# Kernel tuning notes

Measured on AMD Instinct MI355X. Metric: run time of the kernel, lower is better.

Reference implementation:

```python
import jax, jax.numpy as jnp
import numpy as np

B, L, D, N = 32, 2048, 1024, 16
N_ITERS = 4
EPS = 1e-8
RMS_EPS = 1e-6
H = 2 * D  # SwiGLU hidden


def setup_inputs() -> dict:
    key = jax.random.key(0)
    ks = jax.random.split(key, 16)
    w = lambda i, shape: jax.random.normal(ks[i], shape, dtype=jnp.float32) * 0.02
    return {
        "encoder_output": jax.random.normal(ks[0], (B, L, D), dtype=jnp.float32),
        "slots_noise": jax.random.normal(ks[1], (B, N, D), dtype=jnp.float32),
        "slots_mu": w(2, (1, 1, D)),
        "slots_sigma": jnp.abs(w(3, (1, 1, D))),
        "g_in": jnp.ones((D,), jnp.float32),     # norm_input.weight
        "g_slots": jnp.ones((D,), jnp.float32),  # norm_slots.weight
        "Wq": w(4, (D, D)),   # torch Linear weight layout (out, in)
        "Wk": w(5, (D, D)),
        "Wv": w(6, (D, D)),
        "w1": w(7, (H, D)),
        "w2": w(8, (H, D)),
        "w3": w(9, (D, H)),
        "W_ih": w(10, (3 * D, D)),  # GRUCell weight_ih (r,z,n stacked)
        "W_hh": w(11, (3 * D, D)),
        "b_ih": jnp.zeros((3 * D,), jnp.float32),
        "b_hh": jnp.zeros((3 * D,), jnp.float32),
    }


def _rmsnorm(x, g):
    var = jnp.mean(x * x, axis=-1, keepdims=True)
    return x * jax.lax.rsqrt(var + RMS_EPS) * g


def _gru_cell(x, h, W_ih, W_hh, b_ih, b_hh):
    # torch.nn.GRUCell: gates ordered (r, z, n)
    gi = x @ W_ih.T + b_ih   # [..., 3D]
    gh = h @ W_hh.T + b_hh
    gi_r, gi_z, gi_n = jnp.split(gi, 3, axis=-1)
    gh_r, gh_z, gh_n = jnp.split(gh, 3, axis=-1)
    r = jax.nn.sigmoid(gi_r + gh_r)
    z = jax.nn.sigmoid(gi_z + gh_z)
    n = jnp.tanh(gi_n + r * gh_n)
    return (1.0 - z) * n + z * h


def reference(encoder_output, slots_noise, slots_mu, slots_sigma, g_in, g_slots,
              Wq, Wk, Wv, w1, w2, w3, W_ih, W_hh, b_ih, b_hh):
    d = encoder_output.shape[-1]
    scale = d ** (-0.5)

    inputs = _rmsnorm(encoder_output, g_in)          # [B, L, D]
    k = inputs @ Wk.T                                # [B, L, D]
    v = inputs @ Wv.T                                # [B, L, D]

    slots = slots_mu + slots_sigma * slots_noise     # [B, N, D]

    for _ in range(N_ITERS):
        slots_prev = slots
        s = _rmsnorm(slots, g_slots)                 # [B, N, D]
        q = s @ Wq.T                                 # [B, N, D]
        dots = jnp.einsum('bnd,bld->bnl', q, k) * scale   # [B, N, L]
        attn = jax.nn.softmax(dots, axis=1)          # competitive softmax over slots
        updates = jnp.einsum('bnl,bld->bnd', attn + EPS, v)     # [B, N, D]
        updates = updates / (jnp.sum(attn, axis=-1, keepdims=True) + EPS)
        # SwiGLU
        updates = (jax.nn.silu(updates @ w1.T) * (updates @ w2.T)) @ w3.T
        slots = _gru_cell(updates, slots_prev, W_ih, W_hh, b_ih, b_hh)
    return slots
```

## Files before the change

### kernel.cpp

```cpp
#include <hip/hip_runtime.h>
#include <hip/hip_bf16.h>
#include <stdint.h>


typedef __bf16 bf16;
typedef __bf16 bf16x2 __attribute__((ext_vector_type(2)));
typedef __bf16 bf16x4 __attribute__((ext_vector_type(4)));
typedef __bf16 bf16x8 __attribute__((ext_vector_type(8)));
typedef float  f32x4  __attribute__((ext_vector_type(4)));

#define MFMA16(a,b,c) __builtin_amdgcn_mfma_f32_16x16x32_bf16((a),(b),(c),0,0,0)

__device__ __forceinline__ void gload16(const void* g, void* l) {
  __builtin_amdgcn_global_load_lds((__attribute__((address_space(1))) const void*)g,
                                   (__attribute__((address_space(3))) void*)l, 16, 0, 0);
}

template<int OUT_F32>
__global__ __launch_bounds__(256, 4)
void gemm_bt64(const bf16* __restrict__ A0, const bf16* __restrict__ B0, void* __restrict__ C0,
               const bf16* __restrict__ A1, const bf16* __restrict__ B1, void* __restrict__ C1,
               int N, int K, float* zbuf)
{
  if (zbuf != nullptr && blockIdx.x == 0 && blockIdx.y == 0 && blockIdx.z == 0) {
    zbuf[threadIdx.x] = 0.f;
    zbuf[threadIdx.x + 256] = 0.f;
  }
  const bf16* A = blockIdx.z ? A1 : A0;
  const bf16* B = blockIdx.z ? B1 : B0;
  void* C = blockIdx.z ? C1 : C0;
  __shared__ __align__(16) bf16 As[64 * 64];
  __shared__ __align__(16) bf16 Bs[64 * 64];
  const int tid = threadIdx.x, wave = tid >> 6, lane = tid & 63;
  const int wm = wave >> 1, wn = wave & 1;
  const int brow = blockIdx.y * 64, bcol = blockIdx.x * 64;
  const int r8 = lane >> 3, c8 = (lane & 7) * 8;
  const int cl = lane & 15, rh = lane >> 4;
  f32x4 acc[2][2] = {};

  for (int k0 = 0; k0 < K; k0 += 64) {
    __syncthreads();
    gload16(A + (size_t)(brow + wave * 16 + r8) * K + k0 + c8,     &As[(wave * 16) * 64]);
    gload16(A + (size_t)(brow + wave * 16 + 8 + r8) * K + k0 + c8, &As[(wave * 16 + 8) * 64]);
    gload16(B + (size_t)(bcol + wave * 16 + r8) * K + k0 + c8,     &Bs[(wave * 16) * 64]);
    gload16(B + (size_t)(bcol + wave * 16 + 8 + r8) * K + k0 + c8, &Bs[(wave * 16 + 8) * 64]);
    __syncthreads();
#pragma unroll
    for (int kk = 0; kk < 2; ++kk) {
      bf16x8 af[2], bfv[2];
#pragma unroll
      for (int m = 0; m < 2; ++m)
        af[m] = *(const bf16x8*)&As[(wm * 32 + m * 16 + cl) * 64 + kk * 32 + rh * 8];
#pragma unroll
      for (int n = 0; n < 2; ++n)
        bfv[n] = *(const bf16x8*)&Bs[(wn * 32 + n * 16 + cl) * 64 + kk * 32 + rh * 8];
#pragma unroll
      for (int m = 0; m < 2; ++m)
#pragma unroll
        for (int n = 0; n < 2; ++n)
          acc[m][n] = MFMA16(af[m], bfv[n], acc[m][n]);
    }
  }
#pragma unroll
  for (int m = 0; m < 2; ++m)
#pragma unroll
    for (int n = 0; n < 2; ++n) {
      int row0 = brow + wm * 32 + m * 16 + rh * 4;
      int col  = bcol + wn * 32 + n * 16 + cl;
#pragma unroll
      for (int r = 0; r < 4; ++r) {
        if (OUT_F32) ((float*)C)[(size_t)(row0 + r) * N + col] = acc[m][n][r];
        else         ((bf16*)C)[(size_t)(row0 + r) * N + col] = (bf16)acc[m][n][r];
      }
    }
}

__global__ __launch_bounds__(256, 4)
void gemm_swiglu(const bf16* __restrict__ A, const bf16* __restrict__ B12, bf16* __restrict__ G)
{
  __shared__ __align__(16) bf16 As[64 * 64];
  __shared__ __align__(16) bf16 B1s[64 * 64];
  __shared__ __align__(16) bf16 B2s[64 * 64];
  const int tid = threadIdx.x, wave = tid >> 6, lane = tid & 63;
  const int wm = wave >> 1, wn = wave & 1;
  const int brow = blockIdx.y * 64, bcol = blockIdx.x * 64;
  const int r8 = lane >> 3, c8 = (lane & 7) * 8;
  const int cl = lane & 15, rh = lane >> 4;
  f32x4 acc1[2][2] = {}, acc2[2][2] = {};

  for (int k0 = 0; k0 < 1024; k0 += 64) {
    __syncthreads();
    gload16(A   + (size_t)(brow + wave * 16 + r8) * 1024 + k0 + c8,            &As[(wave * 16) * 64]);
    gload16(A   + (size_t)(brow + wave * 16 + 8 + r8) * 1024 + k0 + c8,        &As[(wave * 16 + 8) * 64]);
    gload16(B12 + (size_t)(bcol + wave * 16 + r8) * 1024 + k0 + c8,            &B1s[(wave * 16) * 64]);
    gload16(B12 + (size_t)(bcol + wave * 16 + 8 + r8) * 1024 + k0 + c8,        &B1s[(wave * 16 + 8) * 64]);
    gload16(B12 + (size_t)(2048 + bcol + wave * 16 + r8) * 1024 + k0 + c8,     &B2s[(wave * 16) * 64]);
    gload16(B12 + (size_t)(2048 + bcol + wave * 16 + 8 + r8) * 1024 + k0 + c8, &B2s[(wave * 16 + 8) * 64]);
    __syncthreads();
#pragma unroll
    for (int kk = 0; kk < 2; ++kk) {
      bf16x8 af[2], b1v[2], b2v[2];
#pragma unroll
      for (int m = 0; m < 2; ++m)
        af[m] = *(const bf16x8*)&As[(wm * 32 + m * 16 + cl) * 64 + kk * 32 + rh * 8];
#pragma unroll
      for (int n = 0; n < 2; ++n) {
        b1v[n] = *(const bf16x8*)&B1s[(wn * 32 + n * 16 + cl) * 64 + kk * 32 + rh * 8];
        b2v[n] = *(const bf16x8*)&B2s[(wn * 32 + n * 16 + cl) * 64 + kk * 32 + rh * 8];
      }
#pragma unroll
      for (int m = 0; m < 2; ++m)
#pragma unroll
        for (int n = 0; n < 2; ++n) {
          acc1[m][n] = MFMA16(af[m], b1v[n], acc1[m][n]);
          acc2[m][n] = MFMA16(af[m], b2v[n], acc2[m][n]);
        }
    }
  }
#pragma unroll
  for (int m = 0; m < 2; ++m)
#pragma unroll
    for (int n = 0; n < 2; ++n) {
      int row0 = brow + wm * 32 + m * 16 + rh * 4;
      int col  = bcol + wn * 32 + n * 16 + cl;
#pragma unroll
      for (int r = 0; r < 4; ++r) {
        float h1 = acc1[m][n][r], h2 = acc2[m][n][r];
        G[(size_t)(row0 + r) * 2048 + col] = (bf16)(h1 / (1.f + __expf(-h1)) * h2);
      }
    }
}

__global__ __launch_bounds__(256, 2)
void fused_attn(const bf16* __restrict__ qm, const bf16* __restrict__ x,
                float* __restrict__ part, float* __restrict__ attn_sum)
{
  extern __shared__ __align__(16) char smem[];
  char* ss  = smem;
  char* ksl = smem + 32768;
  float* p_lds = (float*)(smem + 65536);

  const int lc = blockIdx.x, b = blockIdx.y;
  const int tid = threadIdx.x, wave = tid >> 6, lane = tid & 63;
  const int cl = lane & 15, rh = lane >> 4;

  const bf16* sb = qm + (size_t)b * 16 * 1024;
  {
    const int c16 = tid & 127, row2 = tid >> 7;
#pragma unroll
    for (int i = 0; i < 8; ++i) {
      int row = i * 2 + row2;
      int colb = (c16 * 16) ^ ((row & 7) << 4);
      gload16(sb + row * 1024 + colb / 2, ss + i * 4096 + wave * 1024);
    }
  }

  const bf16* kb = x + ((size_t)b * 2048 + lc * 128) * 1024;
  const int ksw  = ((lane & 7) ^ ((lane >> 3) & 7)) * 8;
  const int krow = wave * 8 + (lane >> 3);

#define STAGE_KS(KT) {                                                            \
    char* d_ = ksl + ((KT) & 1) * 16384;                                          \
    _Pragma("unroll")                                                             \
    for (int i = 0; i < 4; ++i)                                                   \
      gload16(kb + (size_t)(i * 32 + krow) * 1024 + (KT) * 64 + ksw,              \
              d_ + (i * 32 + wave * 8) * 128);                                    \
  }

  f32x4 acc[2] = {};
  STAGE_KS(0)
  for (int kt = 0; kt < 16; ++kt) {
    if (kt < 15) { STAGE_KS(kt + 1) }
    __builtin_amdgcn_sched_barrier(0);
    if (kt < 15) asm volatile("s_waitcnt vmcnt(4)" ::: "memory");
    else         asm volatile("s_waitcnt vmcnt(0)" ::: "memory");
    __builtin_amdgcn_sched_barrier(0);
    __builtin_amdgcn_s_barrier();
    const char* sbuf = ksl + (kt & 1) * 16384;
#pragma unroll
    for (int kk = 0; kk < 2; ++kk) {
      bf16x8 af = *(const bf16x8*)(ss + cl * 2048 +
                    ((kt * 128 + kk * 64 + rh * 16) ^ ((cl & 7) << 4)));
#pragma unroll
      for (int n = 0; n < 2; ++n) {
        int row = wave * 32 + n * 16 + cl;
        bf16x8 bfv = *(const bf16x8*)(sbuf + row * 128 +
                      ((kk * 64 + rh * 16) ^ ((row & 7) << 4)));
        acc[n] = MFMA16(af, bfv, acc[n]);
      }
    }
    __builtin_amdgcn_s_barrier();
    __builtin_amdgcn_sched_barrier(0);
  }
#undef STAGE_KS

  const float scale = 0.03125f;
  float rs[4] = {0.f, 0.f, 0.f, 0.f};
#pragma unroll
  for (int n = 0; n < 2; ++n) {
    float xv[4];
#pragma unroll
    for (int r = 0; r < 4; ++r) xv[r] = acc[n][r] * scale;
    float mx = fmaxf(fmaxf(xv[0], xv[1]), fmaxf(xv[2], xv[3]));
    mx = fmaxf(mx, __shfl_xor(mx, 16));
    mx = fmaxf(mx, __shfl_xor(mx, 32));
    float e[4], sm = 0.f;
#pragma unroll
    for (int r = 0; r < 4; ++r) { e[r] = __expf(xv[r] - mx); sm += e[r]; }
    sm += __shfl_xor(sm, 16);
    sm += __shfl_xor(sm, 32);
    float inv = 1.f / sm;
    f32x4 pk;
#pragma unroll
    for (int r = 0; r < 4; ++r) { float av = e[r] * inv; rs[r] += av; pk[r] = av; }
    int ll = wave * 32 + n * 16 + cl;
    *(f32x4*)&p_lds[ll * 20 + rh * 4] = pk;
  }
#pragma unroll
  for (int off = 1; off < 16; off <<= 1) {
#pragma unroll
    for (int r = 0; r < 4; ++r) rs[r] += __shfl_xor(rs[r], off);
  }
  if (cl == 0) {
#pragma unroll
    for (int r = 0; r < 4; ++r) atomicAdd(&attn_sum[b * 16 + rh * 4 + r], rs[r]);
  }
  __syncthreads();

  const bf16* vb = x + ((size_t)b * 2048 + lc * 128) * 1024 + tid * 4;
  float pacc[16][4] = {};
  for (int l = 0; l < 128; ++l) {
    bf16x4 vv = *(const bf16x4*)(vb + (size_t)l * 1024);
    float vf0 = (float)vv[0], vf1 = (float)vv[1], vf2 = (float)vv[2], vf3 = (float)vv[3];
    float pv[16];
    *(f32x4*)&pv[0]  = *(const f32x4*)&p_lds[l * 20];
    *(f32x4*)&pv[4]  = *(const f32x4*)&p_lds[l * 20 + 4];
    *(f32x4*)&pv[8]  = *(const f32x4*)&p_lds[l * 20 + 8];
    *(f32x4*)&pv[12] = *(const f32x4*)&p_lds[l * 20 + 12];
#pragma unroll
    for (int n = 0; n < 16; ++n) {
      pacc[n][0] += pv[n] * vf0; pacc[n][1] += pv[n] * vf1;
      pacc[n][2] += pv[n] * vf2; pacc[n][3] += pv[n] * vf3;
    }
  }
  float* pb = part + ((size_t)(lc * 32 + b) * 16) * 1024 + tid * 4;
#pragma unroll
  for (int n = 0; n < 16; ++n)
    *(f32x4*)(pb + (size_t)n * 1024) = *(f32x4*)&pacc[n][0];
}

__global__ void updates_finalize(const float* __restrict__ part, const float* __restrict__ attn_sum,
                                 bf16* __restrict__ updraw)
{
  int idx = blockIdx.x * 256 + threadIdx.x;
  int m = idx >> 10;
  float sm = 0.f;
#pragma unroll
  for (int ls = 0; ls < 16; ++ls) sm += part[idx + (size_t)ls * 524288];
  updraw[idx] = (bf16)(sm / (attn_sum[m] + 1e-8f));
}

__global__ __launch_bounds__(256)
void gru_pw_fused(const float* __restrict__ gi, const float* __restrict__ gh,
                  const float* __restrict__ bih, const float* __restrict__ bhh,
                  const float* __restrict__ g_sl,
                  float* __restrict__ slots, bf16* __restrict__ slots_bf,
                  bf16* __restrict__ s_bf, float* __restrict__ outp)
{
  const int m = blockIdx.x, tid = threadIdx.x;
  const int d0 = tid * 4;
  const size_t base = (size_t)m * 3072 + d0;
  f32x4 gir = *(const f32x4*)(gi + base),        ghr = *(const f32x4*)(gh + base);
  f32x4 giz = *(const f32x4*)(gi + base + 1024), ghz = *(const f32x4*)(gh + base + 1024);
  f32x4 gin = *(const f32x4*)(gi + base + 2048), ghn = *(const f32x4*)(gh + base + 2048);
  f32x4 br  = *(const f32x4*)(bih + d0),        bhr = *(const f32x4*)(bhh + d0);
  f32x4 bz  = *(const f32x4*)(bih + 1024 + d0), bhz = *(const f32x4*)(bhh + 1024 + d0);
  f32x4 bn  = *(const f32x4*)(bih + 2048 + d0), bhn = *(const f32x4*)(bhh + 2048 + d0);
  f32x4 h   = *(const f32x4*)(slots + (size_t)m * 1024 + d0);
  float o[4]; float ssum = 0.f;
#pragma unroll
  for (int j = 0; j < 4; ++j) {
    float r  = gir[j] + br[j] + ghr[j] + bhr[j];
    float z  = giz[j] + bz[j] + ghz[j] + bhz[j];
    float nn = gin[j] + bn[j];
    float hn = ghn[j] + bhn[j];
    r = 1.f / (1.f + expf(-r));
    z = 1.f / (1.f + expf(-z));
    nn = tanhf(nn + r * hn);
    o[j] = (1.f - z) * nn + z * h[j];
    ssum += o[j] * o[j];
  }
#pragma unroll
  for (int off = 32; off; off >>= 1) ssum += __shfl_xor(ssum, off);
  __shared__ float red[4];
  if ((tid & 63) == 0) red[tid >> 6] = ssum;
  __syncthreads();
  float tot = red[0] + red[1] + red[2] + red[3];
  float rsc = rsqrtf(tot * (1.f / 1024.f) + 1e-6f);
  f32x4 gv = *(const f32x4*)(g_sl + d0);
  f32x4 of; bf16x4 ob, sb;
#pragma unroll
  for (int j = 0; j < 4; ++j) { of[j] = o[j]; ob[j] = (bf16)o[j]; sb[j] = (bf16)(o[j] * rsc * gv[j]); }
  *(f32x4*)(slots + (size_t)m * 1024 + d0) = of;
  *(f32x4*)(outp  + (size_t)m * 1024 + d0) = of;
  *(bf16x4*)(slots_bf + (size_t)m * 1024 + d0) = ob;
  *(bf16x4*)(s_bf     + (size_t)m * 1024 + d0) = sb;
}

__global__ __launch_bounds__(256)
void init_slots_fused(const float* __restrict__ noise, const float* __restrict__ mu,
                      const float* __restrict__ sigma, const float* __restrict__ g_sl,
                      float* __restrict__ slots, bf16* __restrict__ slots_bf,
                      bf16* __restrict__ s_bf)
{
  const int m = blockIdx.x, tid = threadIdx.x;
  const int d0 = tid * 4;
  f32x4 nz = *(const f32x4*)(noise + (size_t)m * 1024 + d0);
  f32x4 mv = *(const f32x4*)(mu + d0);
  f32x4 sg = *(const f32x4*)(sigma + d0);
  float o[4]; float ssum = 0.f;
#pragma unroll
  for (int j = 0; j < 4; ++j) { o[j] = mv[j] + sg[j] * nz[j]; ssum += o[j] * o[j]; }
#pragma unroll
  for (int off = 32; off; off >>= 1) ssum += __shfl_xor(ssum, off);
  __shared__ float red[4];
  if ((tid & 63) == 0) red[tid >> 6] = ssum;
  __syncthreads();
  float tot = red[0] + red[1] + red[2] + red[3];
  float rsc = rsqrtf(tot * (1.f / 1024.f) + 1e-6f);
  f32x4 gv = *(const f32x4*)(g_sl + d0);
  f32x4 of; bf16x4 ob, sb;
#pragma unroll
  for (int j = 0; j < 4; ++j) { of[j] = o[j]; ob[j] = (bf16)o[j]; sb[j] = (bf16)(o[j] * rsc * gv[j]); }
  *(f32x4*)(slots + (size_t)m * 1024 + d0) = of;
  *(bf16x4*)(slots_bf + (size_t)m * 1024 + d0) = ob;
  *(bf16x4*)(s_bf     + (size_t)m * 1024 + d0) = sb;
}

__global__ __launch_bounds__(256)
void rmsnorm_cast(const float* __restrict__ x, const float* __restrict__ g, bf16* __restrict__ y)
{
  const int row = blockIdx.x, tid = threadIdx.x;
  float4 xv = ((const float4*)(x + (size_t)row * 1024))[tid];
  float ss = xv.x * xv.x + xv.y * xv.y + xv.z * xv.z + xv.w * xv.w;
#pragma unroll
  for (int off = 32; off; off >>= 1) ss += __shfl_xor(ss, off);
  __shared__ float red[4];
  if ((tid & 63) == 0) red[tid >> 6] = ss;
  __syncthreads();
  float tot = red[0] + red[1] + red[2] + red[3];
  float rs = rsqrtf(tot * (1.f / 1024.f) + 1e-6f);
  float4 gv = ((const float4*)g)[tid];
  bf16x4 o;
  o[0] = (bf16)(xv.x * rs * gv.x); o[1] = (bf16)(xv.y * rs * gv.y);
  o[2] = (bf16)(xv.z * rs * gv.z); o[3] = (bf16)(xv.w * rs * gv.w);
  *(bf16x4*)(y + (size_t)row * 1024 + tid * 4) = o;
}

__global__ __launch_bounds__(256)
void transpose_cast(const float* __restrict__ in, bf16* __restrict__ out)
{
  __shared__ float tile[32][33];
  const int bx = blockIdx.x * 32, by = blockIdx.y * 32;
  const int tx = threadIdx.x & 31, ty = threadIdx.x >> 5;
#pragma unroll
  for (int i = 0; i < 32; i += 8)
    tile[ty + i][tx] = in[(size_t)(by + ty + i) * 1024 + bx + tx];
  __syncthreads();
#pragma unroll
  for (int i = 0; i < 32; i += 8)
    out[(size_t)(bx + ty + i) * 1024 + by + tx] = (bf16)tile[tx][ty + i];
}

__global__ void cast_bf16_x4(const float* __restrict__ x, bf16* __restrict__ y)
{
  int i = (blockIdx.x * 256 + threadIdx.x) * 4;
  float4 v = *(const float4*)(x + i);
  bf16x4 o; o[0] = (bf16)v.x; o[1] = (bf16)v.y; o[2] = (bf16)v.z; o[3] = (bf16)v.w;
  *(bf16x4*)(y + i) = o;
}

extern "C" void kernel_launch(void* const* d_in, const int* in_sizes, int n_in,
                              void* d_out, int out_size, void* d_ws, size_t ws_size,
                              hipStream_t stream)
{
  const float* enc    = (const float*)d_in[0];
  const float* noise  = (const float*)d_in[1];
  const float* mu     = (const float*)d_in[2];
  const float* sigma  = (const float*)d_in[3];
  const float* g_in   = (const float*)d_in[4];
  const float* g_sl   = (const float*)d_in[5];
  const float* Wq     = (const float*)d_in[6];
  const float* Wk     = (const float*)d_in[7];
  const float* Wv     = (const float*)d_in[8];
  const float* w1     = (const float*)d_in[9];
  const float* w2     = (const float*)d_in[10];
  const float* w3     = (const float*)d_in[11];
  const float* Wih    = (const float*)d_in[12];
  const float* Whh    = (const float*)d_in[13];
  const float* bih    = (const float*)d_in[14];
  const float* bhh    = (const float*)d_in[15];

  char* p = (char*)d_ws;
  auto alloc = [&](size_t bytes) { char* r = p; p += (bytes + 255) & ~(size_t)255; return (void*)r; };

  bf16* inputs  = (bf16*)alloc((size_t)32 * 2048 * 1024 * 2);
  bf16* qm_w    = (bf16*)alloc((size_t)1024 * 1024 * 2);
  bf16* wv_b    = (bf16*)alloc((size_t)1024 * 1024 * 2);
  bf16* wqT_b   = (bf16*)alloc((size_t)1024 * 1024 * 2);
  bf16* wkT_b   = (bf16*)alloc((size_t)1024 * 1024 * 2);
  bf16* w12_b   = (bf16*)alloc((size_t)4096 * 1024 * 2);
  bf16* w3_b    = (bf16*)alloc((size_t)1024 * 2048 * 2);
  bf16* wih_b   = (bf16*)alloc((size_t)3072 * 1024 * 2);
  bf16* whh_b   = (bf16*)alloc((size_t)3072 * 1024 * 2);
  float* slots  = (float*)alloc(512 * 1024 * 4);
  bf16* slots_bf= (bf16*)alloc(512 * 1024 * 2);
  bf16* s_bf    = (bf16*)alloc(512 * 1024 * 2);
  bf16* qm_bf   = (bf16*)alloc(512 * 1024 * 2);
  float* attn_sum = (float*)alloc(32 * 16 * 4);
  float* part   = (float*)alloc((size_t)16 * 512 * 1024 * 4);
  bf16* updraw  = (bf16*)alloc(512 * 1024 * 2);
  bf16* upd_bf  = (bf16*)alloc(512 * 1024 * 2);
  bf16* g_bf    = (bf16*)alloc((size_t)512 * 2048 * 2);
  bf16* swout   = (bf16*)alloc(512 * 1024 * 2);
  float* gif    = (float*)alloc((size_t)512 * 3072 * 4);
  float* ghf    = (float*)alloc((size_t)512 * 3072 * 4);

  transpose_cast<<<dim3(32, 32), 256, 0, stream>>>(Wq, wqT_b);
  transpose_cast<<<dim3(32, 32), 256, 0, stream>>>(Wk, wkT_b);
  gemm_bt64<0><<<dim3(16, 16, 1), 256, 0, stream>>>(wkT_b, wqT_b, qm_w, wkT_b, wqT_b, qm_w, 1024, 1024, nullptr);
  cast_bf16_x4<<<1024, 256, 0, stream>>>(Wv, wv_b);
  cast_bf16_x4<<<2048, 256, 0, stream>>>(w1, w12_b);
  cast_bf16_x4<<<2048, 256, 0, stream>>>(w2, w12_b + (size_t)2048 * 1024);
  cast_bf16_x4<<<2048, 256, 0, stream>>>(w3, w3_b);
  cast_bf16_x4<<<3072, 256, 0, stream>>>(Wih, wih_b);
  cast_bf16_x4<<<3072, 256, 0, stream>>>(Whh, whh_b);

  rmsnorm_cast<<<65536, 256, 0, stream>>>(enc, g_in, inputs);
  init_slots_fused<<<512, 256, 0, stream>>>(noise, mu, sigma, g_sl, slots, slots_bf, s_bf);

  hipFuncSetAttribute(reinterpret_cast<const void*>(fused_attn),
                      hipFuncAttributeMaxDynamicSharedMemorySize, 75776);

  for (int it = 0; it < 4; ++it) {
    gemm_bt64<0><<<dim3(16, 8, 1), 256, 0, stream>>>(s_bf, qm_w, qm_bf, s_bf, qm_w, qm_bf, 1024, 1024, attn_sum);
    fused_attn<<<dim3(16, 32), 256, 75776, stream>>>(qm_bf, inputs, part, attn_sum);
    updates_finalize<<<2048, 256, 0, stream>>>(part, attn_sum, updraw);
    gemm_bt64<0><<<dim3(16, 8, 1), 256, 0, stream>>>(updraw, wv_b, upd_bf, updraw, wv_b, upd_bf, 1024, 1024, nullptr);
    gemm_swiglu<<<dim3(32, 8), 256, 0, stream>>>(upd_bf, w12_b, g_bf);
    gemm_bt64<0><<<dim3(16, 8, 1), 256, 0, stream>>>(g_bf, w3_b, swout, g_bf, w3_b, swout, 1024, 2048, nullptr);
    gemm_bt64<1><<<dim3(48, 8, 2), 256, 0, stream>>>(swout, wih_b, gif, slots_bf, whh_b, ghf, 3072, 1024, nullptr);
    float* outp = (it == 3) ? (float*)d_out : slots;
    gru_pw_fused<<<512, 256, 0, stream>>>(gif, ghf, bih, bhh, g_sl, slots, slots_bf, s_bf, outp);
  }
}
```

Baseline: 796.6 us.

## Fold Wv and w3 into neighbouring weights and double-buffer GEMM LDS

Precomputes the weight products (w1;w2)·Wv and W_ih·w3 once per call so each iteration drops two small GEMM launches: the Wv projection merges into the SwiGLU GEMM, and the w3 projection merges into the GRU input GEMM with K=2048. Both GEMM kernels also switch to double-buffered LDS tiles, prefetching the next K-tile while computing the current one, with explicit vmcnt waits and barriers. The cost is three extra setup GEMMs, more per-iteration K work in the GRU GEMM, fewer blocks per CU for the SwiGLU kernel, and changed bf16 rounding because the weights are pre-multiplied.

New measurement: 735.3 us. -7.7%, faster.

```diff
diff --git a/kernel.cpp b/kernel.cpp
--- a/kernel.cpp
+++ b/kernel.cpp
@@ -4,7 +4,6 @@
 
 
 typedef __bf16 bf16;
-typedef __bf16 bf16x2 __attribute__((ext_vector_type(2)));
 typedef __bf16 bf16x4 __attribute__((ext_vector_type(4)));
 typedef __bf16 bf16x8 __attribute__((ext_vector_type(8)));
 typedef float  f32x4  __attribute__((ext_vector_type(4)));
@@ -20,7 +19,7 @@
 __global__ __launch_bounds__(256, 4)
 void gemm_bt64(const bf16* __restrict__ A0, const bf16* __restrict__ B0, void* __restrict__ C0,
                const bf16* __restrict__ A1, const bf16* __restrict__ B1, void* __restrict__ C1,
-               int N, int K, float* zbuf)
+               int N, int K0, int K1, float* zbuf)
 {
   if (zbuf != nullptr && blockIdx.x == 0 && blockIdx.y == 0 && blockIdx.z == 0) {
     zbuf[threadIdx.x] = 0.f;
@@ -29,8 +28,9 @@
   const bf16* A = blockIdx.z ? A1 : A0;
   const bf16* B = blockIdx.z ? B1 : B0;
   void* C = blockIdx.z ? C1 : C0;
-  __shared__ __align__(16) bf16 As[64 * 64];
-  __shared__ __align__(16) bf16 Bs[64 * 64];
+  const int K = blockIdx.z ? K1 : K0;
+  __shared__ __align__(16) bf16 As[2][64 * 64];
+  __shared__ __align__(16) bf16 Bs[2][64 * 64];
   const int tid = threadIdx.x, wave = tid >> 6, lane = tid & 63;
   const int wm = wave >> 1, wn = wave & 1;
   const int brow = blockIdx.y * 64, bcol = blockIdx.x * 64;
@@ -38,29 +38,53 @@
   const int cl = lane & 15, rh = lane >> 4;
   f32x4 acc[2][2] = {};
 
-  for (int k0 = 0; k0 < K; k0 += 64) {
-    __syncthreads();
-    gload16(A + (size_t)(brow + wave * 16 + r8) * K + k0 + c8,     &As[(wave * 16) * 64]);
-    gload16(A + (size_t)(brow + wave * 16 + 8 + r8) * K + k0 + c8, &As[(wave * 16 + 8) * 64]);
-    gload16(B + (size_t)(bcol + wave * 16 + r8) * K + k0 + c8,     &Bs[(wave * 16) * 64]);
-    gload16(B + (size_t)(bcol + wave * 16 + 8 + r8) * K + k0 + c8, &Bs[(wave * 16 + 8) * 64]);
-    __syncthreads();
+  const bf16* pa0 = A + (size_t)(brow + wave * 16 + r8) * K + c8;
+  const bf16* pa1 = A + (size_t)(brow + wave * 16 + 8 + r8) * K + c8;
+  const bf16* pb0 = B + (size_t)(bcol + wave * 16 + r8) * K + c8;
+  const bf16* pb1 = B + (size_t)(bcol + wave * 16 + 8 + r8) * K + c8;
+
+#define ST64(T) {                                                   \
+    int k0_ = (T) * 64, s_ = (T) & 1;                               \
+    gload16(pa0 + k0_, &As[s_][(wave * 16) * 64]);                  \
+    gload16(pa1 + k0_, &As[s_][(wave * 16 + 8) * 64]);              \
+    gload16(pb0 + k0_, &Bs[s_][(wave * 16) * 64]);                  \
+    gload16(pb1 + k0_, &Bs[s_][(wave * 16 + 8) * 64]);              \
+  }
+
+  const int nt = K >> 6;
+  ST64(0)
+  for (int t = 0; t < nt; ++t) {
+    if (t + 1 < nt) {
+      ST64(t + 1)
+      asm volatile("s_waitcnt vmcnt(4)" ::: "memory");
+    } else {
+      asm volatile("s_waitcnt vmcnt(0)" ::: "memory");
+    }
+    __builtin_amdgcn_sched_barrier(0);
+    __builtin_amdgcn_s_barrier();
+    __builtin_amdgcn_sched_barrier(0);
+    const int s = t & 1;
 #pragma unroll
     for (int kk = 0; kk < 2; ++kk) {
       bf16x8 af[2], bfv[2];
 #pragma unroll
       for (int m = 0; m < 2; ++m)
-        af[m] = *(const bf16x8*)&As[(wm * 32 + m * 16 + cl) * 64 + kk * 32 + rh * 8];
+        af[m] = *(const bf16x8*)&As[s][(wm * 32 + m * 16 + cl) * 64 + kk * 32 + rh * 8];
 #pragma unroll
       for (int n = 0; n < 2; ++n)
-        bfv[n] = *(const bf16x8*)&Bs[(wn * 32 + n * 16 + cl) * 64 + kk * 32 + rh * 8];
+        bfv[n] = *(const bf16x8*)&Bs[s][(wn * 32 + n * 16 + cl) * 64 + kk * 32 + rh * 8];
 #pragma unroll
       for (int m = 0; m < 2; ++m)
 #pragma unroll
         for (int n = 0; n < 2; ++n)
           acc[m][n] = MFMA16(af[m], bfv[n], acc[m][n]);
     }
-  }
+    __builtin_amdgcn_sched_barrier(0);
+    __builtin_amdgcn_s_barrier();
+    __builtin_amdgcn_sched_barrier(0);
+  }
+#undef ST64
+
 #pragma unroll
   for (int m = 0; m < 2; ++m)
 #pragma unroll
@@ -75,12 +99,12 @@
     }
 }
 
-__global__ __launch_bounds__(256, 4)
+__global__ __launch_bounds__(256, 3)
 void gemm_swiglu(const bf16* __restrict__ A, const bf16* __restrict__ B12, bf16* __restrict__ G)
 {
-  __shared__ __align__(16) bf16 As[64 * 64];
-  __shared__ __align__(16) bf16 B1s[64 * 64];
-  __shared__ __align__(16) bf16 B2s[64 * 64];
+  __shared__ __align__(16) bf16 As[2][64 * 64];
+  __shared__ __align__(16) bf16 B1s[2][64 * 64];
+  __shared__ __align__(16) bf16 B2s[2][64 * 64];
   const int tid = threadIdx.x, wave = tid >> 6, lane = tid & 63;
   const int wm = wave >> 1, wn = wave & 1;
   const int brow = blockIdx.y * 64, bcol = blockIdx.x * 64;
@@ -88,25 +112,45 @@
   const int cl = lane & 15, rh = lane >> 4;
   f32x4 acc1[2][2] = {}, acc2[2][2] = {};
 
-  for (int k0 = 0; k0 < 1024; k0 += 64) {
-    __syncthreads();
-    gload16(A   + (size_t)(brow + wave * 16 + r8) * 1024 + k0 + c8,            &As[(wave * 16) * 64]);
-    gload16(A   + (size_t)(brow + wave * 16 + 8 + r8) * 1024 + k0 + c8,        &As[(wave * 16 + 8) * 64]);
-    gload16(B12 + (size_t)(bcol + wave * 16 + r8) * 1024 + k0 + c8,            &B1s[(wave * 16) * 64]);
-    gload16(B12 + (size_t)(bcol + wave * 16 + 8 + r8) * 1024 + k0 + c8,        &B1s[(wave * 16 + 8) * 64]);
-    gload16(B12 + (size_t)(2048 + bcol + wave * 16 + r8) * 1024 + k0 + c8,     &B2s[(wave * 16) * 64]);
-    gload16(B12 + (size_t)(2048 + bcol + wave * 16 + 8 + r8) * 1024 + k0 + c8, &B2s[(wave * 16 + 8) * 64]);
-    __syncthreads();
+  const bf16* pa0 = A   + (size_t)(brow + wave * 16 + r8) * 1024 + c8;
+  const bf16* pa1 = A   + (size_t)(brow + wave * 16 + 8 + r8) * 1024 + c8;
+  const bf16* p10 = B12 + (size_t)(bcol + wave * 16 + r8) * 1024 + c8;
+  const bf16* p11 = B12 + (size_t)(bcol + wave * 16 + 8 + r8) * 1024 + c8;
+  const bf16* p20 = B12 + (size_t)(2048 + bcol + wave * 16 + r8) * 1024 + c8;
+  const bf16* p21 = B12 + (size_t)(2048 + bcol + wave * 16 + 8 + r8) * 1024 + c8;
+
+#define STSW(T) {                                                   \
+    int k0_ = (T) * 64, s_ = (T) & 1;                               \
+    gload16(pa0 + k0_, &As[s_][(wave * 16) * 64]);                  \
+    gload16(pa1 + k0_, &As[s_][(wave * 16 + 8) * 64]);              \
+    gload16(p10 + k0_, &B1s[s_][(wave * 16) * 64]);                 \
+    gload16(p11 + k0_, &B1s[s_][(wave * 16 + 8) * 64]);             \
+    gload16(p20 + k0_, &B2s[s_][(wave * 16) * 64]);                 \
+    gload16(p21 + k0_, &B2s[s_][(wave * 16 + 8) * 64]);             \
+  }
+
+  STSW(0)
+  for (int t = 0; t < 16; ++t) {
+    if (t < 15) {
+      STSW(t + 1)
+      asm volatile("s_waitcnt vmcnt(6)" ::: "memory");
+    } else {
+      asm volatile("s_waitcnt vmcnt(0)" ::: "memory");
+    }
+    __builtin_amdgcn_sched_barrier(0);
+    __builtin_amdgcn_s_barrier();
+    __builtin_amdgcn_sched_barrier(0);
+    const int s = t & 1;
 #pragma unroll
     for (int kk = 0; kk < 2; ++kk) {
       bf16x8 af[2], b1v[2], b2v[2];
 #pragma unroll
       for (int m = 0; m < 2; ++m)
-        af[m] = *(const bf16x8*)&As[(wm * 32 + m * 16 + cl) * 64 + kk * 32 + rh * 8];
+        af[m] = *(const bf16x8*)&As[s][(wm * 32 + m * 16 + cl) * 64 + kk * 32 + rh * 8];
 #pragma unroll
       for (int n = 0; n < 2; ++n) {
-        b1v[n] = *(const bf16x8*)&B1s[(wn * 32 + n * 16 + cl) * 64 + kk * 32 + rh * 8];
-        b2v[n] = *(const bf16x8*)&B2s[(wn * 32 + n * 16 + cl) * 64 + kk * 32 + rh * 8];
+        b1v[n] = *(const bf16x8*)&B1s[s][(wn * 32 + n * 16 + cl) * 64 + kk * 32 + rh * 8];
+        b2v[n] = *(const bf16x8*)&B2s[s][(wn * 32 + n * 16 + cl) * 64 + kk * 32 + rh * 8];
       }
 #pragma unroll
       for (int m = 0; m < 2; ++m)
@@ -116,7 +160,12 @@
           acc2[m][n] = MFMA16(af[m], b2v[n], acc2[m][n]);
         }
     }
-  }
+    __builtin_amdgcn_sched_barrier(0);
+    __builtin_amdgcn_s_barrier();
+    __builtin_amdgcn_sched_barrier(0);
+  }
+#undef STSW
+
 #pragma unroll
   for (int m = 0; m < 2; ++m)
 #pragma unroll
@@ -358,18 +407,18 @@
 }
 
 __global__ __launch_bounds__(256)
-void transpose_cast(const float* __restrict__ in, bf16* __restrict__ out)
+void transpose_cast(const float* __restrict__ in, bf16* __restrict__ out, int R, int C)
 {
   __shared__ float tile[32][33];
   const int bx = blockIdx.x * 32, by = blockIdx.y * 32;
   const int tx = threadIdx.x & 31, ty = threadIdx.x >> 5;
 #pragma unroll
   for (int i = 0; i < 32; i += 8)
-    tile[ty + i][tx] = in[(size_t)(by + ty + i) * 1024 + bx + tx];
+    tile[ty + i][tx] = in[(size_t)(by + ty + i) * C + bx + tx];
   __syncthreads();
 #pragma unroll
   for (int i = 0; i < 32; i += 8)
-    out[(size_t)(bx + ty + i) * 1024 + by + tx] = (bf16)tile[tx][ty + i];
+    out[(size_t)(bx + ty + i) * R + by + tx] = (bf16)tile[tx][ty + i];
 }
 
 __global__ void cast_bf16_x4(const float* __restrict__ x, bf16* __restrict__ y)
@@ -406,12 +455,14 @@
 
   bf16* inputs  = (bf16*)alloc((size_t)32 * 2048 * 1024 * 2);
   bf16* qm_w    = (bf16*)alloc((size_t)1024 * 1024 * 2);
-  bf16* wv_b    = (bf16*)alloc((size_t)1024 * 1024 * 2);
   bf16* wqT_b   = (bf16*)alloc((size_t)1024 * 1024 * 2);
   bf16* wkT_b   = (bf16*)alloc((size_t)1024 * 1024 * 2);
-  bf16* w12_b   = (bf16*)alloc((size_t)4096 * 1024 * 2);
-  bf16* w3_b    = (bf16*)alloc((size_t)1024 * 2048 * 2);
-  bf16* wih_b   = (bf16*)alloc((size_t)3072 * 1024 * 2);
+  bf16* wvT_b   = (bf16*)alloc((size_t)1024 * 1024 * 2);
+  bf16* w3T_b   = (bf16*)alloc((size_t)2048 * 1024 * 2);
+  bf16* w12_bf  = (bf16*)alloc((size_t)4096 * 1024 * 2);
+  bf16* w12v    = (bf16*)alloc((size_t)4096 * 1024 * 2);
+  bf16* wih_bf  = (bf16*)alloc((size_t)3072 * 1024 * 2);
+  bf16* wih3_b  = (bf16*)alloc((size_t)3072 * 2048 * 2);
   bf16* whh_b   = (bf16*)alloc((size_t)3072 * 1024 * 2);
   float* slots  = (float*)alloc(512 * 1024 * 4);
   bf16* slots_bf= (bf16*)alloc(512 * 1024 * 2);
@@ -420,21 +471,24 @@
   float* attn_sum = (float*)alloc(32 * 16 * 4);
   float* part   = (float*)alloc((size_t)16 * 512 * 1024 * 4);
   bf16* updraw  = (bf16*)alloc(512 * 1024 * 2);
-  bf16* upd_bf  = (bf16*)alloc(512 * 1024 * 2);
   bf16* g_bf    = (bf16*)alloc((size_t)512 * 2048 * 2);
-  bf16* swout   = (bf16*)alloc(512 * 1024 * 2);
   float* gif    = (float*)alloc((size_t)512 * 3072 * 4);
   float* ghf    = (float*)alloc((size_t)512 * 3072 * 4);
 
-  transpose_cast<<<dim3(32, 32), 256, 0, stream>>>(Wq, wqT_b);
-  transpose_cast<<<dim3(32, 32), 256, 0, stream>>>(Wk, wkT_b);
-  gemm_bt64<0><<<dim3(16, 16, 1), 256, 0, stream>>>(wkT_b, wqT_b, qm_w, wkT_b, wqT_b, qm_w, 1024, 1024, nullptr);
-  cast_bf16_x4<<<1024, 256, 0, stream>>>(Wv, wv_b);
-  cast_bf16_x4<<<2048, 256, 0, stream>>>(w1, w12_b);
-  cast_bf16_x4<<<2048, 256, 0, stream>>>(w2, w12_b + (size_t)2048 * 1024);
-  cast_bf16_x4<<<2048, 256, 0, stream>>>(w3, w3_b);
-  cast_bf16_x4<<<3072, 256, 0, stream>>>(Wih, wih_b);
+  transpose_cast<<<dim3(32, 32), 256, 0, stream>>>(Wq, wqT_b, 1024, 1024);
+  transpose_cast<<<dim3(32, 32), 256, 0, stream>>>(Wk, wkT_b, 1024, 1024);
+  transpose_cast<<<dim3(32, 32), 256, 0, stream>>>(Wv, wvT_b, 1024, 1024);
+  transpose_cast<<<dim3(64, 32), 256, 0, stream>>>(w3, w3T_b, 1024, 2048);
+  cast_bf16_x4<<<2048, 256, 0, stream>>>(w1, w12_bf);
+  cast_bf16_x4<<<2048, 256, 0, stream>>>(w2, w12_bf + (size_t)2048 * 1024);
+  cast_bf16_x4<<<3072, 256, 0, stream>>>(Wih, wih_bf);
   cast_bf16_x4<<<3072, 256, 0, stream>>>(Whh, whh_b);
+  gemm_bt64<0><<<dim3(16, 16, 1), 256, 0, stream>>>(wkT_b, wqT_b, qm_w, wkT_b, wqT_b, qm_w,
+                                                    1024, 1024, 1024, nullptr);
+  gemm_bt64<0><<<dim3(16, 64, 1), 256, 0, stream>>>(w12_bf, wvT_b, w12v, w12_bf, wvT_b, w12v,
+                                                    1024, 1024, 1024, nullptr);
+  gemm_bt64<0><<<dim3(32, 48, 1), 256, 0, stream>>>(wih_bf, w3T_b, wih3_b, wih_bf, w3T_b, wih3_b,
+                                                    2048, 1024, 1024, nullptr);
 
   rmsnorm_cast<<<65536, 256, 0, stream>>>(enc, g_in, inputs);
   init_slots_fused<<<512, 256, 0, stream>>>(noise, mu, sigma, g_sl, slots, slots_bf, s_bf);
@@ -443,13 +497,13 @@
                       hipFuncAttributeMaxDynamicSharedMemorySize, 75776);
 
   for (int it = 0; it < 4; ++it) {
-    gemm_bt64<0><<<dim3(16, 8, 1), 256, 0, stream>>>(s_bf, qm_w, qm_bf, s_bf, qm_w, qm_bf, 1024, 1024, attn_sum);
+    gemm_bt64<0><<<dim3(16, 8, 1), 256, 0, stream>>>(s_bf, qm_w, qm_bf, s_bf, qm_w, qm_bf,
+                                                     1024, 1024, 1024, attn_sum);
     fused_attn<<<dim3(16, 32), 256, 75776, stream>>>(qm_bf, inputs, part, attn_sum);
     updates_finalize<<<2048, 256, 0, stream>>>(part, attn_sum, updraw);
-    gemm_bt64<0><<<dim3(16, 8, 1), 256, 0, stream>>>(updraw, wv_b, upd_bf, updraw, wv_b, upd_bf, 1024, 1024, nullptr);
-    gemm_swiglu<<<dim3(32, 8), 256, 0, stream>>>(upd_bf, w12_b, g_bf);
-    gemm_bt64<0><<<dim3(16, 8, 1), 256, 0, stream>>>(g_bf, w3_b, swout, g_bf, w3_b, swout, 1024, 2048, nullptr);
-    gemm_bt64<1><<<dim3(48, 8, 2), 256, 0, stream>>>(swout, wih_b, gif, slots_bf, whh_b, ghf, 3072, 1024, nullptr);
+    gemm_swiglu<<<dim3(32, 8), 256, 0, stream>>>(updraw, w12v, g_bf);
+    gemm_bt64<1><<<dim3(48, 8, 2), 256, 0, stream>>>(g_bf, wih3_b, gif, slots_bf, whh_b, ghf,
+                                                     3072, 2048, 1024, nullptr);
     float* outp = (it == 3) ? (float*)d_out : slots;
     gru_pw_fused<<<512, 256, 0, stream>>>(gif, ghf, bih, bhh, g_sl, slots, slots_bf, s_bf, outp);
   }
```
